# Kernel tuning notes

Hardware: AMD Instinct MI355X
Metric: run time of the kernel (lower is better)

## Reference

```python
import jax, jax.numpy as jnp
import numpy as np
import math

B, SEQ_LEN, LABEL_LEN, PRED_LEN = 32, 512, 256, 256
D_MODEL, N_HEADS, D_FF = 512, 8, 2048
ENC_IN, DEC_IN, C_OUT, MARK = 21, 21, 21, 4
MA_K, E_LAYERS, D_LAYERS, FACTOR = 25, 2, 1, 1
DEC_LEN = LABEL_LEN + PRED_LEN


def moving_mean(x, k):
    # replicate-pad front/back then avg-pool(kernel=k, stride=1); x: [B,L,C]
    pad = (k - 1) // 2
    xp = jnp.concatenate([jnp.repeat(x[:, :1], pad, axis=1), x,
                          jnp.repeat(x[:, -1:], pad, axis=1)], axis=1)
    cs = jnp.cumsum(xp, axis=1)
    cs = jnp.concatenate([jnp.zeros_like(cs[:, :1]), cs], axis=1)
    return (cs[:, k:] - cs[:, :-k]) / k


def series_decomp(x):
    trend = moving_mean(x, MA_K)
    return x - trend, trend


def circ_conv3(x, W):
    # circular-padded Conv1d kernel=3, no bias; x: [B,L,Cin], W: [3,Cin,Cout]
    xp = jnp.concatenate([x[:, -1:], x, x[:, :1]], axis=1)
    return xp[:, :-2] @ W[0] + xp[:, 1:-1] @ W[1] + xp[:, 2:] @ W[2]


def pos_embed(L, d):
    pos = jnp.arange(L, dtype=jnp.float32)[:, None]
    div = jnp.exp(jnp.arange(0, d, 2, dtype=jnp.float32) * (-math.log(10000.0) / d))
    pe = jnp.zeros((L, d), jnp.float32)
    pe = pe.at[:, 0::2].set(jnp.sin(pos * div)).at[:, 1::2].set(jnp.cos(pos * div))
    return pe


def data_embed(x, x_mark, val_W, time_W):
    # TokenEmbedding (circular conv) + TimeFeatureEmbedding (linear) + PositionalEmbedding
    return circ_conv3(x, val_W) + x_mark @ time_W + pos_embed(x.shape[1], D_MODEL)[None]


def autocorrelation(q, k, v):
    # q: [B,L,H,E]; k,v: [B,S,H,E]  -> [B,L,H,E]
    Bq, L, H, E = q.shape
    S = k.shape[1]
    if L > S:
        pad = jnp.zeros((Bq, L - S, H, E), q.dtype)
        k = jnp.concatenate([k, pad], axis=1)
        v = jnp.concatenate([v, pad], axis=1)
    else:
        k, v = k[:, :L], v[:, :L]
    qf = jnp.fft.rfft(q.transpose(0, 2, 3, 1), axis=-1)
    kf = jnp.fft.rfft(k.transpose(0, 2, 3, 1), axis=-1)
    corr = jnp.fft.irfft(qf * jnp.conj(kf), n=L, axis=-1)   # [B,H,E,L]
    vals = v.transpose(0, 2, 3, 1)                          # [B,H,E,L]
    top_k = int(FACTOR * math.log(L))
    mean_corr = corr.mean(axis=(1, 2))                      # [B,L]
    weights, delay = jax.lax.top_k(mean_corr, top_k)        # [B,K]
    w = jax.nn.softmax(weights, axis=-1)
    # gather from doubled values == circular shift by delay
    idx = (jnp.arange(L)[None, None, :] + delay[:, :, None]) % L   # [B,K,L]
    pat = jnp.take_along_axis(vals[:, None], idx[:, :, None, None, :], axis=-1)  # [B,K,H,E,L]
    agg = jnp.einsum('bkhel,bk->bhel', pat, w)
    return agg.transpose(0, 3, 1, 2)


def ac_layer(qx, kx, vx, Wq, Wk, Wv, Wo):
    Bq, L, D = qx.shape
    dk = D // N_HEADS
    q = (qx @ Wq).reshape(Bq, L, N_HEADS, dk)
    k = (kx @ Wk).reshape(Bq, kx.shape[1], N_HEADS, dk)
    v = (vx @ Wv).reshape(Bq, vx.shape[1], N_HEADS, dk)
    return autocorrelation(q, k, v).reshape(Bq, L, D) @ Wo


def ffn(x, W1, W2):
    # Conv1d kernel=1 (no bias) pair == pointwise MLP
    return jax.nn.gelu(x @ W1, approximate=False) @ W2


def seasonal_ln(x, g, b):
    mu = x.mean(-1, keepdims=True)
    var = ((x - mu) ** 2).mean(-1, keepdims=True)
    xh = (x - mu) / jnp.sqrt(var + 1e-5) * g + b
    return xh - xh.mean(axis=1, keepdims=True)


def encoder_layer(x, Wq, Wk, Wv, Wo, W1, W2):
    x = x + ac_layer(x, x, x, Wq, Wk, Wv, Wo)
    x, _ = series_decomp(x)
    y = ffn(x, W1, W2)
    x, _ = series_decomp(x + y)
    return x


def decoder_layer(x, cross, sWq, sWk, sWv, sWo, cWq, cWk, cWv, cWo, W1, W2, trend_W):
    x = x + ac_layer(x, x, x, sWq, sWk, sWv, sWo)
    x, t1 = series_decomp(x)
    x = x + ac_layer(x, cross, cross, cWq, cWk, cWv, cWo)
    x, t2 = series_decomp(x)
    y = ffn(x, W1, W2)
    x, t3 = series_decomp(x + y)
    residual_trend = circ_conv3(t1 + t2 + t3, trend_W)   # [B,L,C_OUT]
    return x, residual_trend


def _forward(x_enc, x_mark_enc, x_dec, x_mark_dec,
             enc_val_W, enc_time_W, enc_Wq, enc_Wk, enc_Wv, enc_Wo, enc_W1, enc_W2,
             enc_norm_g, enc_norm_b, dec_val_W, dec_time_W,
             dec_sWq, dec_sWk, dec_sWv, dec_sWo, dec_cWq, dec_cWk, dec_cWv, dec_cWo,
             dec_W1, dec_W2, dec_trend_W, dec_norm_g, dec_norm_b, proj_W, proj_b):
    mean = jnp.repeat(x_enc.mean(axis=1, keepdims=True), PRED_LEN, axis=1)
    zeros = jnp.zeros((x_dec.shape[0], PRED_LEN, x_dec.shape[2]), x_enc.dtype)
    seasonal_init, trend_init = series_decomp(x_enc)
    trend_init = jnp.concatenate([trend_init[:, -LABEL_LEN:], mean], axis=1)
    seasonal_init = jnp.concatenate([seasonal_init[:, -LABEL_LEN:], zeros], axis=1)
    enc = data_embed(x_enc, x_mark_enc, enc_val_W, enc_time_W)
    for i in range(E_LAYERS):
        enc = encoder_layer(enc, enc_Wq[i], enc_Wk[i], enc_Wv[i], enc_Wo[i], enc_W1[i], enc_W2[i])
    enc = seasonal_ln(enc, enc_norm_g, enc_norm_b)
    dec = data_embed(seasonal_init, x_mark_dec, dec_val_W, dec_time_W)
    trend = trend_init
    for i in range(D_LAYERS):
        dec, rt = decoder_layer(dec, enc, dec_sWq[i], dec_sWk[i], dec_sWv[i], dec_sWo[i],
                                dec_cWq[i], dec_cWk[i], dec_cWv[i], dec_cWo[i],
                                dec_W1[i], dec_W2[i], dec_trend_W[i])
        trend = trend + rt
    dec = seasonal_ln(dec, dec_norm_g, dec_norm_b)
    dec_out = dec @ proj_W + proj_b + trend
    return dec_out[:, -PRED_LEN:]


def setup_inputs() -> dict:
    key = jax.random.key(0)
    it = iter(jax.random.split(key, 40))
    def rn(shape, s=1.0):
        return jax.random.normal(next(it), shape, jnp.float32) * s
    W = 0.02
    return {
        'x_enc': rn((B, SEQ_LEN, ENC_IN)),
        'x_mark_enc': rn((B, SEQ_LEN, MARK)),
        'x_dec': rn((B, DEC_LEN, DEC_IN)),
        'x_mark_dec': rn((B, DEC_LEN, MARK)),
        'enc_val_W': rn((3, ENC_IN, D_MODEL), W),
        'enc_time_W': rn((MARK, D_MODEL), W),
        'enc_Wq': rn((E_LAYERS, D_MODEL, D_MODEL), W),
        'enc_Wk': rn((E_LAYERS, D_MODEL, D_MODEL), W),
        'enc_Wv': rn((E_LAYERS, D_MODEL, D_MODEL), W),
        'enc_Wo': rn((E_LAYERS, D_MODEL, D_MODEL), W),
        'enc_W1': rn((E_LAYERS, D_MODEL, D_FF), W),
        'enc_W2': rn((E_LAYERS, D_FF, D_MODEL), W),
        'enc_norm_g': jnp.ones((D_MODEL,), jnp.float32),
        'enc_norm_b': jnp.zeros((D_MODEL,), jnp.float32),
        'dec_val_W': rn((3, DEC_IN, D_MODEL), W),
        'dec_time_W': rn((MARK, D_MODEL), W),
        'dec_sWq': rn((D_LAYERS, D_MODEL, D_MODEL), W),
        'dec_sWk': rn((D_LAYERS, D_MODEL, D_MODEL), W),
        'dec_sWv': rn((D_LAYERS, D_MODEL, D_MODEL), W),
        'dec_sWo': rn((D_LAYERS, D_MODEL, D_MODEL), W),
        'dec_cWq': rn((D_LAYERS, D_MODEL, D_MODEL), W),
        'dec_cWk': rn((D_LAYERS, D_MODEL, D_MODEL), W),
        'dec_cWv': rn((D_LAYERS, D_MODEL, D_MODEL), W),
        'dec_cWo': rn((D_LAYERS, D_MODEL, D_MODEL), W),
        'dec_W1': rn((D_LAYERS, D_MODEL, D_FF), W),
        'dec_W2': rn((D_LAYERS, D_FF, D_MODEL), W),
        'dec_trend_W': rn((D_LAYERS, 3, D_MODEL, C_OUT), W),
        'dec_norm_g': jnp.ones((D_MODEL,), jnp.float32),
        'dec_norm_b': jnp.zeros((D_MODEL,), jnp.float32),
        'proj_W': rn((D_MODEL, C_OUT), W),
        'proj_b': jnp.zeros((C_OUT,), jnp.float32),
    }


def reference(x_enc, x_mark_enc, x_dec, x_mark_dec,
              enc_val_W, enc_time_W, enc_Wq, enc_Wk, enc_Wv, enc_Wo, enc_W1, enc_W2,
              enc_norm_g, enc_norm_b, dec_val_W, dec_time_W,
              dec_sWq, dec_sWk, dec_sWv, dec_sWo, dec_cWq, dec_cWk, dec_cWv, dec_cWo,
              dec_W1, dec_W2, dec_trend_W, dec_norm_g, dec_norm_b, proj_W, proj_b):
    return _forward(x_enc, x_mark_enc, x_dec, x_mark_dec,
                    enc_val_W, enc_time_W, enc_Wq, enc_Wk, enc_Wv, enc_Wo, enc_W1, enc_W2,
                    enc_norm_g, enc_norm_b, dec_val_W, dec_time_W,
                    dec_sWq, dec_sWk, dec_sWv, dec_sWo, dec_cWq, dec_cWk, dec_cWv, dec_cWo,
                    dec_W1, dec_W2, dec_trend_W, dec_norm_g, dec_norm_b, proj_W, proj_b)
```

## Files before the change

### kernel.cpp

```cpp
#include <hip/hip_runtime.h>


typedef _Float16 h8 __attribute__((ext_vector_type(8)));
typedef _Float16 h4 __attribute__((ext_vector_type(4)));
typedef float f32x4 __attribute__((ext_vector_type(4)));

struct P12 { const float* p[12]; };
struct P4  { const float* p[4]; };

__device__ __forceinline__ float gelu_f(float x){
    return 0.5f * x * (1.0f + erff(x * 0.70710678118654752f));
}

__device__ __forceinline__ void gl_lds(const _Float16* gp, _Float16* lp) {
    __builtin_amdgcn_global_load_lds(
        (const __attribute__((address_space(1))) void*)gp,
        (__attribute__((address_space(3))) void*)lp, 16, 0, 0);
}

__global__ void zero_k(float* __restrict__ p, long n){
    long i = (long)blockIdx.x * 256 + threadIdx.x;
    if (i < n) p[i] = 0.f;
}

template<int EPI, int OUT>
__global__ __launch_bounds__(256)
void hgemm_k(const _Float16* __restrict__ A, int lda, int loA,
             const _Float16* __restrict__ Bm, int ldb, int loB,
             const float* __restrict__ R, void* __restrict__ Cv,
             int ldc, int loC, int K, int nph, float osc,
             long sA, long sB, long sC)
{
    __shared__ _Float16 As[128 * 64];
    __shared__ _Float16 Bs[128 * 64];
    const int bz = blockIdx.z;
    const int tid = threadIdx.x, lane = tid & 63, w = tid >> 6;
    const int wr = w >> 1, wc = w & 1;
    const _Float16* Ap = A + bz * sA + (long)(blockIdx.y * 128) * lda;
    const _Float16* Bp = Bm + bz * sB + (long)(blockIdx.x * 128) * ldb;

    const int swz = ((lane & 7) ^ ((lane >> 3) & 7)) * 8;
    const int rsub = w * 32 + (lane >> 3);
    const _Float16* ApT = Ap + (long)rsub * lda + swz;
    const _Float16* BpT = Bp + (long)rsub * ldb + swz;
    _Float16* AsT = As + w * 2048;
    _Float16* BsT = Bs + w * 2048;

    const int tpp = K >> 6;
    const int nkt = tpp * nph;
    f32x4 acc[4][4] = {};

    int p = 0, q = 0;
    for (int kt = 0; kt < nkt; ++kt) {
        const int aoff = q * 64 + (p == 2 ? loA : 0);
        const int boff = q * 64 + (p == 1 ? loB : 0);
        __syncthreads();
#pragma unroll
        for (int i = 0; i < 4; i++) {
            gl_lds(ApT + (long)i * 8 * lda + aoff, AsT + i * 512);
            gl_lds(BpT + (long)i * 8 * ldb + boff, BsT + i * 512);
        }
        __syncthreads();
#pragma unroll
        for (int kk = 0; kk < 2; ++kk) {
            h8 af[4], bf[4];
            const int ks = kk * 4 + (lane >> 4);
#pragma unroll
            for (int m = 0; m < 4; m++) {
                int rowa = wr * 64 + m * 16 + (lane & 15);
                af[m] = *(const h8*)(As + rowa * 64 + ((ks ^ (rowa & 7)) * 8));
                int rowb = wc * 64 + m * 16 + (lane & 15);
                bf[m] = *(const h8*)(Bs + rowb * 64 + ((ks ^ (rowb & 7)) * 8));
            }
#pragma unroll
            for (int m = 0; m < 4; m++)
#pragma unroll
                for (int n = 0; n < 4; n++)
                    acc[m][n] = __builtin_amdgcn_mfma_f32_16x16x32_f16(af[m], bf[n], acc[m][n], 0, 0, 0);
        }
        if (++q == tpp) { q = 0; ++p; }
    }

    const int crow0 = blockIdx.y * 128 + wr * 64 + (lane >> 4) * 4;
    const int ccol0 = blockIdx.x * 128 + wc * 64 + (lane & 15);
    if constexpr (OUT == 0) {
        float* Cp = (float*)Cv + (long)bz * sC;
        const float* Rp = (EPI == 1) ? (R + (long)bz * sC) : nullptr;
#pragma unroll
        for (int m = 0; m < 4; m++)
#pragma unroll
            for (int n = 0; n < 4; n++) {
                int col = ccol0 + n * 16;
#pragma unroll
                for (int r2 = 0; r2 < 4; r2++) {
                    long idx = (long)(crow0 + m * 16 + r2) * ldc + col;
                    float v = acc[m][n][r2] * osc;
                    if (EPI == 1) v += Rp[idx];
                    Cp[idx] = v;
                }
            }
    } else if constexpr (OUT == 1) {
        _Float16* Cp = (_Float16*)Cv + (long)bz * sC;
#pragma unroll
        for (int m = 0; m < 4; m++)
#pragma unroll
            for (int n = 0; n < 4; n++) {
                int col = ccol0 + n * 16;
#pragma unroll
                for (int r2 = 0; r2 < 4; r2++) {
                    long base = (long)(crow0 + m * 16 + r2) * ldc + col;
                    float v = acc[m][n][r2] * osc;
                    if (EPI == 2) v = gelu_f(v);
                    _Float16 hi = (_Float16)v;
                    Cp[base] = hi;
                    if (loC >= 0) Cp[base + loC] = (_Float16)(v - (float)hi);
                }
            }
    } else {
        __shared__ float diag[512];
        float* mc = (float*)Cv + (long)bz * sC;
        for (int t = tid; t < 512; t += 256) diag[t] = 0.f;
        __syncthreads();
#pragma unroll
        for (int m = 0; m < 4; m++)
#pragma unroll
            for (int n = 0; n < 4; n++) {
                int col = ccol0 + n * 16;
#pragma unroll
                for (int r2 = 0; r2 < 4; r2++) {
                    int row = crow0 + m * 16 + r2;
                    atomicAdd(&diag[(row - col) & 511], acc[m][n][r2]);
                }
            }
        __syncthreads();
        for (int t = tid; t < 512; t += 256) {
            float v = diag[t];
            if (v != 0.f) atomicAdd(&mc[t], v);
        }
    }
}

__global__ __launch_bounds__(256)
void splitAll_k(P12 ps, _Float16* __restrict__ PA, _Float16* __restrict__ PB)
{
    const int m = blockIdx.y;
    const float* __restrict__ src = ps.p[m];
    _Float16* dst;
    if (m < 4)      dst = PA + (long)(2 * m) * 524288;
    else if (m < 8) dst = PB + (long)(2 * (m - 4)) * 524288;
    else            dst = PB + (long)(2 * (m - 8) + 1) * 524288;
    long t = (long)blockIdx.x * 256 + threadIdx.x;
    long row = t >> 6; int kc = (int)(t & 63) * 8;
    const float4 v0 = *(const float4*)(src + row * 512 + kc);
    const float4 v1 = *(const float4*)(src + row * 512 + kc + 4);
    float vv[8] = {v0.x,v0.y,v0.z,v0.w,v1.x,v1.y,v1.z,v1.w};
    h8 hi, lo;
#pragma unroll
    for (int j = 0; j < 8; j++) {
        float s = vv[j] * 64.f;
        _Float16 h = (_Float16)s;
        hi[j] = h; lo[j] = (_Float16)(s - (float)h);
    }
    *(h8*)(dst + row * 1024 + kc)       = hi;
    *(h8*)(dst + row * 1024 + 512 + kc) = lo;
}

__global__ __launch_bounds__(256)
void convWoAll_k(P4 ps, _Float16* __restrict__ PA)
{
    const int z = blockIdx.z;
    const float* __restrict__ src = ps.p[z];
    _Float16* dst = PA + (long)(2 * z + 1) * 524288;
    __shared__ float t[32][33];
    int k0 = blockIdx.x * 32, n0 = blockIdx.y * 32, tid = threadIdx.x;
#pragma unroll
    for (int i = 0; i < 4; i++) {
        int lin = tid + i * 256; int r = lin >> 5, c = lin & 31;
        t[r][c] = src[(long)(k0 + r) * 512 + n0 + c];
    }
    __syncthreads();
#pragma unroll
    for (int i = 0; i < 4; i++) {
        int lin = tid + i * 256; int n = lin >> 5, k = lin & 31;
        float v = t[k][n] * 64.f;
        _Float16 hi = (_Float16)v;
        long base = (long)(n0 + n) * 1024 + k0 + k;
        dst[base]       = hi;
        dst[base + 512] = (_Float16)(v - (float)hi);
    }
}

__global__ __launch_bounds__(256)
void convW2_k(const float* __restrict__ src, _Float16* __restrict__ dst,
              int N, int K)
{
    __shared__ float t[32][33];
    int k0 = blockIdx.x * 32, n0 = blockIdx.y * 32, tid = threadIdx.x;
#pragma unroll
    for (int i = 0; i < 4; i++) {
        int lin = tid + i * 256; int r = lin >> 5, c = lin & 31;
        t[r][c] = src[(long)(k0 + r) * N + n0 + c];
    }
    __syncthreads();
#pragma unroll
    for (int i = 0; i < 4; i++) {
        int lin = tid + i * 256; int n = lin >> 5, k = lin & 31;
        float v = t[k][n];
        _Float16 hi = (_Float16)v;
        long base = (long)(n0 + n) * 2 * K + k0 + k;
        dst[base]     = hi;
        dst[base + K] = (_Float16)(v - (float)hi);
    }
}

__global__ void convW63_k(const float* __restrict__ W, _Float16* __restrict__ dst)
{
    int i = blockIdx.x * 256 + threadIdx.x;
    int k = i & 511, j = i >> 9;
    float v = (j < 63) ? 64.f * W[(long)(j / 21) * 10752 + (long)k * 21 + (j % 21)] : 0.f;
    _Float16 hi = (_Float16)v;
    dst[(long)j * 1024 + k]       = hi;
    dst[(long)j * 1024 + 512 + k] = (_Float16)(v - (float)hi);
}

__global__ __launch_bounds__(256)
void embed_k(const float* __restrict__ x, const float* __restrict__ mark,
             const float* __restrict__ valW, const float* __restrict__ timeW,
             float* __restrict__ out, _Float16* __restrict__ cat)
{
    const int lg = blockIdx.x, dh = blockIdx.y, b = blockIdx.z;
    const int tid = threadIdx.x;
    const int dd = dh * 256 + tid;
    const int l0 = lg * 8;
    __shared__ float xs[10][21];
    __shared__ float mk[8][4];
    if (tid < 210) {
        int r = tid / 21, c = tid % 21;
        int ll = (l0 - 1 + r + 512) & 511;
        xs[r][c] = x[((long)b * 512 + ll) * 21 + c];
    }
    if (tid >= 224 && tid < 256) {
        int t2 = tid - 224, il = t2 >> 2, m = t2 & 3;
        mk[il][m] = mark[((long)b * 512 + l0 + il) * 4 + m];
    }
    __syncthreads();
    float acc[8];
#pragma unroll
    for (int il = 0; il < 8; il++) acc[il] = 0.f;
    for (int t = 0; t < 3; t++)
        for (int c = 0; c < 21; c++) {
            float w = valW[(t * 21 + c) * 512 + dd];
#pragma unroll
            for (int il = 0; il < 8; il++)
                acc[il] = fmaf(xs[il + t][c], w, acc[il]);
        }
    for (int m = 0; m < 4; m++) {
        float w = timeW[m * 512 + dd];
#pragma unroll
        for (int il = 0; il < 8; il++)
            acc[il] = fmaf(mk[il][m], w, acc[il]);
    }
    const float freq = expf((float)(dd & ~1) * (-9.210340371976184f / 512.0f));
#pragma unroll
    for (int il = 0; il < 8; il++) {
        float ang = (float)(l0 + il) * freq;
        float pe = (dd & 1) ? cosf(ang) : sinf(ang);
        float v = acc[il] + pe;
        long row = (long)b * 512 + l0 + il;
        out[row * 512 + dd] = v;
        _Float16 hi = (_Float16)v;
        cat[row * 1024 + dd]       = hi;
        cat[row * 1024 + 512 + dd] = (_Float16)(v - (float)hi);
    }
}

template<int TREND, int CAT>
__global__ __launch_bounds__(256)
void decompW_k(const float* __restrict__ x, float* __restrict__ out,
               _Float16* __restrict__ cat, _Float16* __restrict__ tsc)
{
    long t = (long)blockIdx.x * 256 + threadIdx.x;
    long rowg = t >> 7; int d4 = (int)(t & 127) * 4;
    int lg = (int)(rowg & 63); long b = rowg >> 6;
    const int l0 = lg * 8;
    const float* xb = x + (b << 18);
    float s[8][4] = {};
    float xo[8][4];
#pragma unroll
    for (int rr = -12; rr <= 19; rr++) {
        int rc = l0 + rr; rc = rc < 0 ? 0 : (rc > 511 ? 511 : rc);
        float4 v = *(const float4*)(xb + ((long)rc << 9) + d4);
        float vv[4] = {v.x, v.y, v.z, v.w};
#pragma unroll
        for (int i = 0; i < 8; i++) {
            if (i >= rr - 12 && i <= rr + 12) {
#pragma unroll
                for (int j = 0; j < 4; j++) s[i][j] += vv[j];
            }
        }
        if (rr >= 0 && rr < 8) {
#pragma unroll
            for (int j = 0; j < 4; j++) xo[rr][j] = vv[j];
        }
    }
#pragma unroll
    for (int i = 0; i < 8; i++) {
        long row = b * 512 + l0 + i;
        float tr[4], ov[4];
#pragma unroll
        for (int j = 0; j < 4; j++) {
            tr[j] = s[i][j] * (1.f / 25.f);
            ov[j] = xo[i][j] - tr[j];
        }
        *(float4*)(out + row * 512 + d4) = make_float4(ov[0], ov[1], ov[2], ov[3]);
        if (CAT) {
            h4 hi, lo;
#pragma unroll
            for (int j = 0; j < 4; j++) {
                _Float16 h = (_Float16)ov[j];
                hi[j] = h; lo[j] = (_Float16)(ov[j] - (float)h);
            }
            *(h4*)(cat + row * 1024 + d4)       = hi;
            *(h4*)(cat + row * 1024 + 512 + d4) = lo;
        }
        if (TREND) {
            _Float16* tp = tsc + row * 1024 + d4;
            if (TREND == 1) {
                h4 th = *(h4*)tp, tl = *(h4*)(tp + 512);
#pragma unroll
                for (int j = 0; j < 4; j++) tr[j] += (float)th[j] + (float)tl[j];
            }
            h4 th2, tl2;
#pragma unroll
            for (int j = 0; j < 4; j++) {
                _Float16 h = (_Float16)tr[j];
                th2[j] = h; tl2[j] = (_Float16)(tr[j] - (float)h);
            }
            *(h4*)tp         = th2;
            *(h4*)(tp + 512) = tl2;
        }
    }
}

__global__ void meanseq_k(const float* __restrict__ x, float* __restrict__ xm, int total)
{
    int i = blockIdx.x * 256 + threadIdx.x;
    if (i >= total) return;
    int c = i % 21, b = i / 21;
    float s = 0.f;
    for (int l = 0; l < 512; l++) s += x[((long)b * 512 + l) * 21 + c];
    xm[i] = s * (1.f / 512.f);
}

__global__ void prep_k(const float* __restrict__ x, const float* __restrict__ xm,
                       float* __restrict__ sinit, float* __restrict__ tinit, int total)
{
    int i = blockIdx.x * 256 + threadIdx.x;
    if (i >= total) return;
    int c = i % 21, l = (i / 21) % 512, b = i / 10752;
    if (l < 256) {
        int lc = 256 + l;
        float s = 0.f;
        for (int j = -12; j <= 12; j++) {
            int ll = lc + j; ll = ll > 511 ? 511 : ll;
            s += x[((long)b * 512 + ll) * 21 + c];
        }
        float t = s * (1.f / 25.f);
        tinit[i] = t;
        sinit[i] = x[((long)b * 512 + lc) * 21 + c] - t;
    } else {
        sinit[i] = 0.f;
        tinit[i] = xm[b * 21 + c];
    }
}

__global__ __launch_bounds__(256)
void topk_k(float* __restrict__ mc, int* __restrict__ delays,
            float* __restrict__ wts)
{
    const float SCL = 1.f / (512.f * 4096.f);
    int b = blockIdx.x, tid = threadIdx.x;
    __shared__ float v[512];
    __shared__ float rv[256];
    __shared__ int   ri[256];
    __shared__ float selv[6];
    v[tid]       = mc[b * 512 + tid]       * SCL;
    v[tid + 256] = mc[b * 512 + tid + 256] * SCL;
    mc[b * 512 + tid] = 0.f;
    mc[b * 512 + tid + 256] = 0.f;
    __syncthreads();
    for (int p = 0; p < 6; p++) {
        float bv = v[tid]; int bi = tid;
        float v2 = v[tid + 256];
        if (v2 > bv) { bv = v2; bi = tid + 256; }
        rv[tid] = bv; ri[tid] = bi;
        __syncthreads();
        for (int s = 128; s > 0; s >>= 1) {
            if (tid < s) {
                float ov = rv[tid + s]; int oi = ri[tid + s];
                if (ov > rv[tid] || (ov == rv[tid] && oi < ri[tid])) {
                    rv[tid] = ov; ri[tid] = oi;
                }
            }
            __syncthreads();
        }
        if (tid == 0) { selv[p] = rv[0]; delays[b * 6 + p] = ri[0]; v[ri[0]] = -3.4e38f; }
        __syncthreads();
    }
    if (tid == 0) {
        float mx = selv[0];
        for (int p = 1; p < 6; p++) mx = fmaxf(mx, selv[p]);
        float e[6], sum = 0.f;
        for (int p = 0; p < 6; p++) { e[p] = expf(selv[p] - mx); sum += e[p]; }
        for (int p = 0; p < 6; p++) wts[b * 6 + p] = e[p] / sum;
    }
}

__global__ __launch_bounds__(256)
void agg2_k(const _Float16* __restrict__ Vc, int vld,
            const int* __restrict__ delays, const float* __restrict__ wts,
            _Float16* __restrict__ out)
{
    long t = (long)blockIdx.x * 256 + threadIdx.x;
    int dc = (int)(t & 63);
    long row = t >> 6;
    int l = (int)(row & 511), b = (int)(row >> 9);
    float s[8] = {};
#pragma unroll
    for (int k = 0; k < 6; k++) {
        int dl = delays[b * 6 + k];
        float wv = wts[b * 6 + k];
        long sr = ((long)b * 512 + ((l + dl) & 511)) * vld + dc * 8;
        h8 hi8 = *(const h8*)(Vc + sr);
#pragma unroll
        for (int j = 0; j < 8; j++)
            s[j] = fmaf(wv, (float)hi8[j], s[j]);
    }
    h8 ho;
#pragma unroll
    for (int j = 0; j < 8; j++) ho[j] = (_Float16)s[j];
    *(h8*)(out + row * 512 + dc * 8) = ho;
}

__global__ __launch_bounds__(256)
void ln_k(const float* __restrict__ x, const float* __restrict__ g,
          const float* __restrict__ be, float* __restrict__ out)
{
    int row = blockIdx.x, tid = threadIdx.x;
    const float* xr = x + ((long)row << 9);
    float v0 = xr[tid], v1 = xr[tid + 256];
    __shared__ float rs[256];
    rs[tid] = v0 + v1; __syncthreads();
    for (int s = 128; s > 0; s >>= 1) { if (tid < s) rs[tid] += rs[tid + s]; __syncthreads(); }
    float mu = rs[0] * (1.f / 512.f);
    __syncthreads();
    float d0 = v0 - mu, d1 = v1 - mu;
    rs[tid] = d0 * d0 + d1 * d1; __syncthreads();
    for (int s = 128; s > 0; s >>= 1) { if (tid < s) rs[tid] += rs[tid + s]; __syncthreads(); }
    float rstd = 1.0f / sqrtf(rs[0] * (1.f / 512.f) + 1e-5f);
    out[((long)row << 9) + tid]       = d0 * rstd * g[tid] + be[tid];
    out[((long)row << 9) + tid + 256] = d1 * rstd * g[tid + 256] + be[tid + 256];
}

__global__ __launch_bounds__(256)
void colsum_k(const float* __restrict__ x, float* __restrict__ cs)
{
    int d = blockIdx.x * 256 + threadIdx.x;
    int b = blockIdx.y;
    const float* xb = x + ((long)b << 18);
    float s = 0.f;
    for (int l = 0; l < 512; l++) s += xb[((long)l << 9) + d];
    cs[((long)b << 9) + d] = s;
}

__global__ __launch_bounds__(256)
void subcolcat_k(const float* __restrict__ x, const float* __restrict__ cs,
                 _Float16* __restrict__ cat)
{
    long t = (long)blockIdx.x * 256 + threadIdx.x;
    long row = t >> 6; int d8 = (int)(t & 63) * 8;
    int b = (int)(row >> 9);
    const float4* c4 = (const float4*)(cs + ((long)b << 9) + d8);
    float4 m0 = c4[0], m1 = c4[1];
    float m[8] = {m0.x,m0.y,m0.z,m0.w,m1.x,m1.y,m1.z,m1.w};
    const float4* xp = (const float4*)(x + row * 512 + d8);
    float4 x0 = xp[0], x1 = xp[1];
    float v[8] = {x0.x,x0.y,x0.z,x0.w,x1.x,x1.y,x1.z,x1.w};
    h8 hi, lo;
#pragma unroll
    for (int j = 0; j < 8; j++) {
        float vv = v[j] - m[j] * (1.f / 512.f);
        _Float16 h = (_Float16)vv;
        hi[j] = h; lo[j] = (_Float16)(vv - (float)h);
    }
    *(h8*)(cat + row * 1024 + d8)       = hi;
    *(h8*)(cat + row * 1024 + 512 + d8) = lo;
}

__global__ void proj_k(const float* __restrict__ x, const float* __restrict__ cs,
                       const float* __restrict__ pw, const float* __restrict__ pb,
                       const float* __restrict__ tinit, const float* __restrict__ H,
                       float* __restrict__ out, int total)
{
    int i = blockIdx.x * 256 + threadIdx.x;
    if (i >= total) return;
    int c = i % 21, l = (i / 21) % 256 + 256, b = i / 5376;
    const float* xr = x + ((long)(b * 512 + l) << 9);
    const float* csb = cs + ((long)b << 9);
    float s = 0.f;
    for (int d = 0; d < 512; d++)
        s = fmaf(xr[d] - csb[d] * (1.f / 512.f), pw[d * 21 + c], s);
    long r = (long)b * 512;
    float trend = tinit[b * 10752 + l * 21 + c]
                + H[(r + ((l + 511) & 511)) * 128 + c]
                + H[(r + l) * 128 + 21 + c]
                + H[(r + ((l + 1) & 511)) * 128 + 42 + c];
    out[i] = s + pb[c] + trend;
}

static void hgemm(int mode, int nph, float osc,
                  const _Float16* A, int lda, int loA,
                  const _Float16* B, int ldb, int loB,
                  const float* R, void* C, int ldc, int loC,
                  int K, int M, int N, int batch,
                  long sA, long sB, long sC, hipStream_t st)
{
    dim3 g(N / 128, M / 128, batch), blk(256);
    switch (mode) {
    case 0:  hgemm_k<0,1><<<g,blk,0,st>>>(A,lda,loA,B,ldb,loB,R,C,ldc,loC,K,nph,osc,sA,sB,sC); break;
    case 2:  hgemm_k<2,1><<<g,blk,0,st>>>(A,lda,loA,B,ldb,loB,R,C,ldc,loC,K,nph,osc,sA,sB,sC); break;
    case 10: hgemm_k<1,0><<<g,blk,0,st>>>(A,lda,loA,B,ldb,loB,R,C,ldc,loC,K,nph,osc,sA,sB,sC); break;
    case 11: hgemm_k<0,0><<<g,blk,0,st>>>(A,lda,loA,B,ldb,loB,R,C,ldc,loC,K,nph,osc,sA,sB,sC); break;
    default: hgemm_k<0,2><<<g,blk,0,st>>>(A,lda,loA,B,ldb,loB,R,C,ldc,loC,K,nph,osc,sA,sB,sC); break;
    }
}

extern "C" void kernel_launch(void* const* d_in, const int* in_sizes, int n_in,
                              void* d_out, int out_size, void* d_ws, size_t ws_size,
                              hipStream_t stream)
{
    const float* x_enc    = (const float*)d_in[0];
    const float* xm_enc   = (const float*)d_in[1];
    const float* xm_dec   = (const float*)d_in[3];
    const float* enc_valW = (const float*)d_in[4];
    const float* enc_timeW= (const float*)d_in[5];
    const float* enc_Wq   = (const float*)d_in[6];
    const float* enc_Wk   = (const float*)d_in[7];
    const float* enc_Wv   = (const float*)d_in[8];
    const float* enc_Wo   = (const float*)d_in[9];
    const float* enc_W1   = (const float*)d_in[10];
    const float* enc_W2   = (const float*)d_in[11];
    const float* enc_g    = (const float*)d_in[12];
    const float* enc_b    = (const float*)d_in[13];
    const float* dec_valW = (const float*)d_in[14];
    const float* dec_timeW= (const float*)d_in[15];
    const float* sWq = (const float*)d_in[16];
    const float* sWk = (const float*)d_in[17];
    const float* sWv = (const float*)d_in[18];
    const float* sWo = (const float*)d_in[19];
    const float* cWq = (const float*)d_in[20];
    const float* cWk = (const float*)d_in[21];
    const float* cWv = (const float*)d_in[22];
    const float* cWo = (const float*)d_in[23];
    const float* dW1 = (const float*)d_in[24];
    const float* dW2 = (const float*)d_in[25];
    const float* dtW = (const float*)d_in[26];
    const float* dec_g = (const float*)d_in[27];
    const float* dec_b = (const float*)d_in[28];
    const float* projW = (const float*)d_in[29];
    const float* projB = (const float*)d_in[30];

    const size_t W_BYTES = 50000000;
    const size_t perB = 8900000;
    int Bc = 32;
    while (Bc > 1 && W_BYTES + (size_t)Bc * perB + (4u << 20) > ws_size) Bc >>= 1;

    char* wp = (char*)d_ws;
    auto alloc = [&](size_t bytes) { char* p = wp; wp += (bytes + 255) & ~(size_t)255; return p; };

    _Float16* Wcat8  = (_Float16*)alloc(8 * 524288 * 2);
    _Float16* encW1C = (_Float16*)alloc(2 * 2097152 * 2);
    _Float16* encW2C = (_Float16*)alloc(2 * 2097152 * 2);
    _Float16* dW1C   = (_Float16*)alloc(2097152 * 2);
    _Float16* dW2C   = (_Float16*)alloc(2097152 * 2);
    _Float16* W63C   = (_Float16*)alloc(131072 * 2);
    _Float16* PA     = (_Float16*)alloc(8 * 524288 * 2);
    _Float16* PB     = (_Float16*)alloc(8 * 524288 * 2);

    const long ROWS = (long)Bc * 512;
    const long NBc  = ROWS * 512;
    float*    X      = (float*)alloc(NBc * 4);
    float*    O      = (float*)alloc(NBc * 4);
    _Float16* TSc    = (_Float16*)alloc(ROWS * 1024 * 2);
    _Float16* cX     = (_Float16*)alloc(ROWS * 1024 * 2);
    _Float16* cAgg   = (_Float16*)alloc(ROWS * 512 * 2);
    _Float16* ENCcat = (_Float16*)alloc(ROWS * 1024 * 2);
    _Float16* bigcat = (_Float16*)alloc(ROWS * 2048 * 2);
    float* H       = (float*)alloc(ROWS * 128 * 4);
    float* sinit   = (float*)alloc((long)Bc * 10752 * 4);
    float* tinit   = (float*)alloc((long)Bc * 10752 * 4);
    float* xmean   = (float*)alloc((long)Bc * 21 * 4);
    float* mc      = (float*)alloc((long)Bc * 512 * 4);
    float* cs      = (float*)alloc((long)Bc * 512 * 4);
    float* wts     = (float*)alloc((long)Bc * 6 * 4);
    int*   delays  = (int*)alloc((long)Bc * 6 * 4);

    dim3 cb(256);
    P12 sp;
    sp.p[0] = enc_Wk;           sp.p[1] = enc_Wk + 262144;
    sp.p[2] = sWk;              sp.p[3] = cWk;
    sp.p[4] = enc_Wq;           sp.p[5] = enc_Wq + 262144;
    sp.p[6] = sWq;              sp.p[7] = cWq;
    sp.p[8] = enc_Wv;           sp.p[9] = enc_Wv + 262144;
    sp.p[10] = sWv;             sp.p[11] = cWv;
    P4 op;
    op.p[0] = enc_Wo;           op.p[1] = enc_Wo + 262144;
    op.p[2] = sWo;              op.p[3] = cWo;
    splitAll_k <<<dim3(128,12), cb, 0, stream>>>(sp, PA, PB);
    convWoAll_k<<<dim3(16,16,4), cb, 0, stream>>>(op, PA);
    hgemm(0, 3, 1.f, PA,1024,512, PB,1024,512, nullptr, Wcat8, 1024, 512,
          512, 512, 512, 8, 524288, 524288, 524288, stream);
    for (int L = 0; L < 2; L++) {
        convW2_k<<<dim3(16,64), cb, 0, stream>>>(enc_W1 + (long)L*1048576, encW1C + (long)L*2097152, 2048, 512);
        convW2_k<<<dim3(64,16), cb, 0, stream>>>(enc_W2 + (long)L*1048576, encW2C + (long)L*2097152, 512, 2048);
    }
    convW2_k<<<dim3(16,64), cb, 0, stream>>>(dW1, dW1C, 2048, 512);
    convW2_k<<<dim3(64,16), cb, 0, stream>>>(dW2, dW2C, 512, 2048);
    convW63_k<<<256, cb, 0, stream>>>(dtW, W63C);

    const int M = (int)ROWS;
    const int t21 = Bc * 10752;
    const int gRows = Bc * 128;
    const int gW = Bc * 32;
    const long sCA = 512 * 1024;
    const float IOS = 1.f / 4096.f;

    zero_k<<<(Bc*512 + 255)/256, 256, 0, stream>>>(mc, Bc*512);

    auto attn = [&](float* Xin, float* Cout, const _Float16* cQ,
                    const _Float16* KVcat, int slot) {
        const _Float16* WqkC_ = Wcat8 + (long)(2*slot)     * 524288;
        const _Float16* WvoC_ = Wcat8 + (long)(2*slot + 1) * 524288;
        hgemm(0, 3, 1.f, cQ,1024,512, WqkC_,1024,512, nullptr, bigcat, 1024, 512,
              512, M, 512, 1, 0,0,0, stream);
        hgemm(20, 3, 1.f, bigcat,1024,512, KVcat,1024,512, nullptr, mc, 0, 0,
              512, 512, 512, Bc, sCA, sCA, 512, stream);
        topk_k<<<Bc, 256, 0, stream>>>(mc, delays, wts);
        agg2_k<<<gRows, 256, 0, stream>>>(KVcat, 1024, delays, wts, cAgg);
        hgemm(10, 1, IOS, cAgg,512,0, WvoC_,1024,512, Xin, Cout, 512, 0,
              512, M, 512, 1, 0,0,0, stream);
    };
    auto ffn = [&](float* Xin, float* Cout, const _Float16* cXin,
                   const _Float16* W1C, const _Float16* W2C) {
        hgemm(2, 1, 1.f, cXin,1024,512, W1C,1024,512, nullptr, bigcat, 2048, -1,
              512, M, 2048, 1, 0,0,0, stream);
        hgemm(10, 1, 1.f, bigcat,2048,0, W2C,4096,2048, Xin, Cout, 512, 0,
              2048, M, 512, 1, 0,0,0, stream);
    };

    for (int b0 = 0; b0 < 32; b0 += Bc) {
        const float* xe  = x_enc  + (long)b0 * 10752;
        const float* mke = xm_enc + (long)b0 * 2048;
        const float* mkd = xm_dec + (long)b0 * 2048;
        float* outp = (float*)d_out + (long)b0 * 5376;

        meanseq_k<<<(Bc*21 + 255)/256, 256, 0, stream>>>(xe, xmean, Bc*21);
        prep_k   <<<(t21 + 255)/256, 256, 0, stream>>>(xe, xmean, sinit, tinit, t21);

        embed_k<<<dim3(64,2,Bc), 256, 0, stream>>>(xe, mke, enc_valW, enc_timeW, X, cX);
        for (int L = 0; L < 2; L++) {
            attn(X, O, cX, cX, L);
            decompW_k<0,1><<<gW, 256, 0, stream>>>(O, X, cX, nullptr);
            ffn(X, O, cX, encW1C + (long)L*2097152, encW2C + (long)L*2097152);
            decompW_k<0,1><<<gW, 256, 0, stream>>>(O, X, cX, nullptr);
        }
        ln_k      <<<Bc*512, 256, 0, stream>>>(X, enc_g, enc_b, O);
        colsum_k  <<<dim3(2,Bc), 256, 0, stream>>>(O, cs);
        subcolcat_k<<<gRows, 256, 0, stream>>>(O, cs, ENCcat);

        embed_k<<<dim3(64,2,Bc), 256, 0, stream>>>(sinit, mkd, dec_valW, dec_timeW, X, cX);

        attn(X, O, cX, cX, 2);
        decompW_k<2,1><<<gW, 256, 0, stream>>>(O, X, cX, TSc);

        attn(X, O, cX, ENCcat, 3);
        decompW_k<1,1><<<gW, 256, 0, stream>>>(O, X, cX, TSc);

        ffn(X, O, cX, dW1C, dW2C);
        decompW_k<1,0><<<gW, 256, 0, stream>>>(O, X, nullptr, TSc);

        hgemm(11, 1, 1.f/64.f, TSc,1024,512, W63C,1024,512, nullptr, H, 128, 0,
              512, M, 128, 1, 0,0,0, stream);
        ln_k      <<<Bc*512, 256, 0, stream>>>(X, dec_g, dec_b, O);
        colsum_k  <<<dim3(2,Bc), 256, 0, stream>>>(O, cs);
        proj_k    <<<(Bc*5376+255)/256, 256, 0, stream>>>(O, cs, projW, projB,
                                                          tinit, H, outp, Bc*5376);
    }
}
```

Baseline: 2.213 ms.

## Store residual stream as split fp16 hi/lo pairs instead of fp32

Replaces the fp32 residual buffers X/O with hi/lo fp16 pair buffers, so GEMM epilogues add the residual from the pair form and write pairs directly, and decomposition and layernorm read pairs. This removes the duplicate fp32 write alongside the fp16 copy and shrinks per-batch workspace, which may allow larger batch chunks. It also replaces the serial per-channel mean kernel with a block-parallel reduction. Precision of the residual is preserved approximately via the hi+lo split.

```diff
diff --git a/kernel.cpp b/kernel.cpp
--- a/kernel.cpp
+++ b/kernel.cpp
@@ -27,7 +27,7 @@
 __global__ __launch_bounds__(256)
 void hgemm_k(const _Float16* __restrict__ A, int lda, int loA,
              const _Float16* __restrict__ Bm, int ldb, int loB,
-             const float* __restrict__ R, void* __restrict__ Cv,
+             const _Float16* __restrict__ Rc, void* __restrict__ Cv,
              int ldc, int loC, int K, int nph, float osc,
              long sA, long sB, long sC)
 {
@@ -85,7 +85,6 @@
     const int ccol0 = blockIdx.x * 128 + wc * 64 + (lane & 15);
     if constexpr (OUT == 0) {
         float* Cp = (float*)Cv + (long)bz * sC;
-        const float* Rp = (EPI == 1) ? (R + (long)bz * sC) : nullptr;
 #pragma unroll
         for (int m = 0; m < 4; m++)
 #pragma unroll
@@ -94,9 +93,7 @@
 #pragma unroll
                 for (int r2 = 0; r2 < 4; r2++) {
                     long idx = (long)(crow0 + m * 16 + r2) * ldc + col;
-                    float v = acc[m][n][r2] * osc;
-                    if (EPI == 1) v += Rp[idx];
-                    Cp[idx] = v;
+                    Cp[idx] = acc[m][n][r2] * osc;
                 }
             }
     } else if constexpr (OUT == 1) {
@@ -108,8 +105,13 @@
                 int col = ccol0 + n * 16;
 #pragma unroll
                 for (int r2 = 0; r2 < 4; r2++) {
-                    long base = (long)(crow0 + m * 16 + r2) * ldc + col;
+                    int row = crow0 + m * 16 + r2;
+                    long base = (long)row * ldc + col;
                     float v = acc[m][n][r2] * osc;
+                    if (EPI == 1) {
+                        long rb = (long)row * 1024 + col;
+                        v += (float)Rc[rb] + (float)Rc[rb + 512];
+                    }
                     if (EPI == 2) v = gelu_f(v);
                     _Float16 hi = (_Float16)v;
                     Cp[base] = hi;
@@ -226,7 +228,7 @@
 __global__ __launch_bounds__(256)
 void embed_k(const float* __restrict__ x, const float* __restrict__ mark,
              const float* __restrict__ valW, const float* __restrict__ timeW,
-             float* __restrict__ out, _Float16* __restrict__ cat)
+             _Float16* __restrict__ cat)
 {
     const int lg = blockIdx.x, dh = blockIdx.y, b = blockIdx.z;
     const int tid = threadIdx.x;
@@ -267,30 +269,32 @@
         float pe = (dd & 1) ? cosf(ang) : sinf(ang);
         float v = acc[il] + pe;
         long row = (long)b * 512 + l0 + il;
-        out[row * 512 + dd] = v;
         _Float16 hi = (_Float16)v;
         cat[row * 1024 + dd]       = hi;
         cat[row * 1024 + 512 + dd] = (_Float16)(v - (float)hi);
     }
 }
 
-template<int TREND, int CAT>
-__global__ __launch_bounds__(256)
-void decompW_k(const float* __restrict__ x, float* __restrict__ out,
-               _Float16* __restrict__ cat, _Float16* __restrict__ tsc)
+template<int TREND>
+__global__ __launch_bounds__(256)
+void decompW_k(const _Float16* __restrict__ xc, _Float16* __restrict__ outc,
+               _Float16* __restrict__ tsc)
 {
     long t = (long)blockIdx.x * 256 + threadIdx.x;
     long rowg = t >> 7; int d4 = (int)(t & 127) * 4;
     int lg = (int)(rowg & 63); long b = rowg >> 6;
     const int l0 = lg * 8;
-    const float* xb = x + (b << 18);
+    const _Float16* xb = xc + (b << 19);
     float s[8][4] = {};
     float xo[8][4];
 #pragma unroll
     for (int rr = -12; rr <= 19; rr++) {
         int rc = l0 + rr; rc = rc < 0 ? 0 : (rc > 511 ? 511 : rc);
-        float4 v = *(const float4*)(xb + ((long)rc << 9) + d4);
-        float vv[4] = {v.x, v.y, v.z, v.w};
+        h4 vh = *(const h4*)(xb + ((long)rc << 10) + d4);
+        h4 vl = *(const h4*)(xb + ((long)rc << 10) + 512 + d4);
+        float vv[4];
+#pragma unroll
+        for (int j = 0; j < 4; j++) vv[j] = (float)vh[j] + (float)vl[j];
 #pragma unroll
         for (int i = 0; i < 8; i++) {
             if (i >= rr - 12 && i <= rr + 12) {
@@ -312,17 +316,14 @@
             tr[j] = s[i][j] * (1.f / 25.f);
             ov[j] = xo[i][j] - tr[j];
         }
-        *(float4*)(out + row * 512 + d4) = make_float4(ov[0], ov[1], ov[2], ov[3]);
-        if (CAT) {
-            h4 hi, lo;
-#pragma unroll
-            for (int j = 0; j < 4; j++) {
-                _Float16 h = (_Float16)ov[j];
-                hi[j] = h; lo[j] = (_Float16)(ov[j] - (float)h);
-            }
-            *(h4*)(cat + row * 1024 + d4)       = hi;
-            *(h4*)(cat + row * 1024 + 512 + d4) = lo;
-        }
+        h4 hi, lo;
+#pragma unroll
+        for (int j = 0; j < 4; j++) {
+            _Float16 h = (_Float16)ov[j];
+            hi[j] = h; lo[j] = (_Float16)(ov[j] - (float)h);
+        }
+        *(h4*)(outc + row * 1024 + d4)       = hi;
+        *(h4*)(outc + row * 1024 + 512 + d4) = lo;
         if (TREND) {
             _Float16* tp = tsc + row * 1024 + d4;
             if (TREND == 1) {
@@ -342,14 +343,26 @@
     }
 }
 
-__global__ void meanseq_k(const float* __restrict__ x, float* __restrict__ xm, int total)
-{
-    int i = blockIdx.x * 256 + threadIdx.x;
-    if (i >= total) return;
-    int c = i % 21, b = i / 21;
-    float s = 0.f;
-    for (int l = 0; l < 512; l++) s += x[((long)b * 512 + l) * 21 + c];
-    xm[i] = s * (1.f / 512.f);
+__global__ __launch_bounds__(512)
+void meanseq2_k(const float* __restrict__ x, float* __restrict__ xm)
+{
+    int b = blockIdx.x, tid = threadIdx.x;
+    __shared__ float sd[504];
+    if (tid < 504) {
+        int c = tid % 21, g = tid / 21;
+        int l0 = g * 22, l1 = l0 + 22 > 512 ? 512 : l0 + 22;
+        const float* xb = x + (long)b * 10752;
+        float s = 0.f;
+        for (int l = l0; l < l1; l++) s += xb[l * 21 + c];
+        sd[tid] = s;
+    }
+    __syncthreads();
+    if (tid < 21) {
+        float t = 0.f;
+#pragma unroll
+        for (int g = 0; g < 24; g++) t += sd[g * 21 + tid];
+        xm[b * 21 + tid] = t * (1.f / 512.f);
+    }
 }
 
 __global__ void prep_k(const float* __restrict__ x, const float* __restrict__ xm,
@@ -443,12 +456,13 @@
 }
 
 __global__ __launch_bounds__(256)
-void ln_k(const float* __restrict__ x, const float* __restrict__ g,
+void ln_k(const _Float16* __restrict__ xc, const float* __restrict__ g,
           const float* __restrict__ be, float* __restrict__ out)
 {
     int row = blockIdx.x, tid = threadIdx.x;
-    const float* xr = x + ((long)row << 9);
-    float v0 = xr[tid], v1 = xr[tid + 256];
+    const _Float16* xr = xc + ((long)row << 10);
+    float v0 = (float)xr[tid]       + (float)xr[tid + 512];
+    float v1 = (float)xr[tid + 256] + (float)xr[tid + 768];
     __shared__ float rs[256];
     rs[tid] = v0 + v1; __syncthreads();
     for (int s = 128; s > 0; s >>= 1) { if (tid < s) rs[tid] += rs[tid + s]; __syncthreads(); }
@@ -521,17 +535,17 @@
 static void hgemm(int mode, int nph, float osc,
                   const _Float16* A, int lda, int loA,
                   const _Float16* B, int ldb, int loB,
-                  const float* R, void* C, int ldc, int loC,
+                  const _Float16* Rc, void* C, int ldc, int loC,
                   int K, int M, int N, int batch,
                   long sA, long sB, long sC, hipStream_t st)
 {
     dim3 g(N / 128, M / 128, batch), blk(256);
     switch (mode) {
-    case 0:  hgemm_k<0,1><<<g,blk,0,st>>>(A,lda,loA,B,ldb,loB,R,C,ldc,loC,K,nph,osc,sA,sB,sC); break;
-    case 2:  hgemm_k<2,1><<<g,blk,0,st>>>(A,lda,loA,B,ldb,loB,R,C,ldc,loC,K,nph,osc,sA,sB,sC); break;
-    case 10: hgemm_k<1,0><<<g,blk,0,st>>>(A,lda,loA,B,ldb,loB,R,C,ldc,loC,K,nph,osc,sA,sB,sC); break;
-    case 11: hgemm_k<0,0><<<g,blk,0,st>>>(A,lda,loA,B,ldb,loB,R,C,ldc,loC,K,nph,osc,sA,sB,sC); break;
-    default: hgemm_k<0,2><<<g,blk,0,st>>>(A,lda,loA,B,ldb,loB,R,C,ldc,loC,K,nph,osc,sA,sB,sC); break;
+    case 0:  hgemm_k<0,1><<<g,blk,0,st>>>(A,lda,loA,B,ldb,loB,Rc,C,ldc,loC,K,nph,osc,sA,sB,sC); break;
+    case 2:  hgemm_k<2,1><<<g,blk,0,st>>>(A,lda,loA,B,ldb,loB,Rc,C,ldc,loC,K,nph,osc,sA,sB,sC); break;
+    case 12: hgemm_k<1,1><<<g,blk,0,st>>>(A,lda,loA,B,ldb,loB,Rc,C,ldc,loC,K,nph,osc,sA,sB,sC); break;
+    case 11: hgemm_k<0,0><<<g,blk,0,st>>>(A,lda,loA,B,ldb,loB,Rc,C,ldc,loC,K,nph,osc,sA,sB,sC); break;
+    default: hgemm_k<0,2><<<g,blk,0,st>>>(A,lda,loA,B,ldb,loB,Rc,C,ldc,loC,K,nph,osc,sA,sB,sC); break;
     }
 }
 
@@ -571,7 +585,7 @@
     const float* projB = (const float*)d_in[30];
 
     const size_t W_BYTES = 50000000;
-    const size_t perB = 8900000;
+    const size_t perB = 8400000;
     int Bc = 32;
     while (Bc > 1 && W_BYTES + (size_t)Bc * perB + (4u << 20) > ws_size) Bc >>= 1;
 
@@ -588,14 +602,13 @@
     _Float16* PB     = (_Float16*)alloc(8 * 524288 * 2);
 
     const long ROWS = (long)Bc * 512;
-    const long NBc  = ROWS * 512;
-    float*    X      = (float*)alloc(NBc * 4);
-    float*    O      = (float*)alloc(NBc * 4);
+    _Float16* cX     = (_Float16*)alloc(ROWS * 1024 * 2);
+    _Float16* cO     = (_Float16*)alloc(ROWS * 1024 * 2);
     _Float16* TSc    = (_Float16*)alloc(ROWS * 1024 * 2);
-    _Float16* cX     = (_Float16*)alloc(ROWS * 1024 * 2);
     _Float16* cAgg   = (_Float16*)alloc(ROWS * 512 * 2);
     _Float16* ENCcat = (_Float16*)alloc(ROWS * 1024 * 2);
     _Float16* bigcat = (_Float16*)alloc(ROWS * 2048 * 2);
+    float* F       = (float*)alloc(ROWS * 512 * 4);
     float* H       = (float*)alloc(ROWS * 128 * 4);
     float* sinit   = (float*)alloc((long)Bc * 10752 * 4);
     float* tinit   = (float*)alloc((long)Bc * 10752 * 4);
@@ -607,15 +620,15 @@
 
     dim3 cb(256);
     P12 sp;
-    sp.p[0] = enc_Wk;           sp.p[1] = enc_Wk + 262144;
-    sp.p[2] = sWk;              sp.p[3] = cWk;
-    sp.p[4] = enc_Wq;           sp.p[5] = enc_Wq + 262144;
-    sp.p[6] = sWq;              sp.p[7] = cWq;
-    sp.p[8] = enc_Wv;           sp.p[9] = enc_Wv + 262144;
-    sp.p[10] = sWv;             sp.p[11] = cWv;
+    sp.p[0] = enc_Wk;  sp.p[1] = enc_Wk + 262144;
+    sp.p[2] = sWk;     sp.p[3] = cWk;
+    sp.p[4] = enc_Wq;  sp.p[5] = enc_Wq + 262144;
+    sp.p[6] = sWq;     sp.p[7] = cWq;
+    sp.p[8] = enc_Wv;  sp.p[9] = enc_Wv + 262144;
+    sp.p[10] = sWv;    sp.p[11] = cWv;
     P4 op;
-    op.p[0] = enc_Wo;           op.p[1] = enc_Wo + 262144;
-    op.p[2] = sWo;              op.p[3] = cWo;
+    op.p[0] = enc_Wo;  op.p[1] = enc_Wo + 262144;
+    op.p[2] = sWo;     op.p[3] = cWo;
     splitAll_k <<<dim3(128,12), cb, 0, stream>>>(sp, PA, PB);
     convWoAll_k<<<dim3(16,16,4), cb, 0, stream>>>(op, PA);
     hgemm(0, 3, 1.f, PA,1024,512, PB,1024,512, nullptr, Wcat8, 1024, 512,
@@ -637,24 +650,24 @@
 
     zero_k<<<(Bc*512 + 255)/256, 256, 0, stream>>>(mc, Bc*512);
 
-    auto attn = [&](float* Xin, float* Cout, const _Float16* cQ,
+    auto attn = [&](const _Float16* cIn, _Float16* cOut,
                     const _Float16* KVcat, int slot) {
         const _Float16* WqkC_ = Wcat8 + (long)(2*slot)     * 524288;
         const _Float16* WvoC_ = Wcat8 + (long)(2*slot + 1) * 524288;
-        hgemm(0, 3, 1.f, cQ,1024,512, WqkC_,1024,512, nullptr, bigcat, 1024, 512,
+        hgemm(0, 3, 1.f, cIn,1024,512, WqkC_,1024,512, nullptr, bigcat, 1024, 512,
               512, M, 512, 1, 0,0,0, stream);
         hgemm(20, 3, 1.f, bigcat,1024,512, KVcat,1024,512, nullptr, mc, 0, 0,
               512, 512, 512, Bc, sCA, sCA, 512, stream);
         topk_k<<<Bc, 256, 0, stream>>>(mc, delays, wts);
         agg2_k<<<gRows, 256, 0, stream>>>(KVcat, 1024, delays, wts, cAgg);
-        hgemm(10, 1, IOS, cAgg,512,0, WvoC_,1024,512, Xin, Cout, 512, 0,
+        hgemm(12, 1, IOS, cAgg,512,0, WvoC_,1024,512, cIn, cOut, 1024, 512,
               512, M, 512, 1, 0,0,0, stream);
     };
-    auto ffn = [&](float* Xin, float* Cout, const _Float16* cXin,
+    auto ffn = [&](const _Float16* cIn, _Float16* cOut,
                    const _Float16* W1C, const _Float16* W2C) {
-        hgemm(2, 1, 1.f, cXin,1024,512, W1C,1024,512, nullptr, bigcat, 2048, -1,
+        hgemm(2, 1, 1.f, cIn,1024,512, W1C,1024,512, nullptr, bigcat, 2048, -1,
               512, M, 2048, 1, 0,0,0, stream);
-        hgemm(10, 1, 1.f, bigcat,2048,0, W2C,4096,2048, Xin, Cout, 512, 0,
+        hgemm(12, 1, 1.f, bigcat,2048,0, W2C,4096,2048, cIn, cOut, 1024, 512,
               2048, M, 512, 1, 0,0,0, stream);
     };
 
@@ -664,36 +677,34 @@
         const float* mkd = xm_dec + (long)b0 * 2048;
         float* outp = (float*)d_out + (long)b0 * 5376;
 
-        meanseq_k<<<(Bc*21 + 255)/256, 256, 0, stream>>>(xe, xmean, Bc*21);
-        prep_k   <<<(t21 + 255)/256, 256, 0, stream>>>(xe, xmean, sinit, tinit, t21);
-
-        embed_k<<<dim3(64,2,Bc), 256, 0, stream>>>(xe, mke, enc_valW, enc_timeW, X, cX);
+        meanseq2_k<<<Bc, 512, 0, stream>>>(xe, xmean);
+        prep_k    <<<(t21 + 255)/256, 256, 0, stream>>>(xe, xmean, sinit, tinit, t21);
+
+        embed_k<<<dim3(64,2,Bc), 256, 0, stream>>>(xe, mke, enc_valW, enc_timeW, cX);
         for (int L = 0; L < 2; L++) {
-            attn(X, O, cX, cX, L);
-            decompW_k<0,1><<<gW, 256, 0, stream>>>(O, X, cX, nullptr);
-            ffn(X, O, cX, encW1C + (long)L*2097152, encW2C + (long)L*2097152);
-            decompW_k<0,1><<<gW, 256, 0, stream>>>(O, X, cX, nullptr);
-        }
-        ln_k      <<<Bc*512, 256, 0, stream>>>(X, enc_g, enc_b, O);
-        colsum_k  <<<dim3(2,Bc), 256, 0, stream>>>(O, cs);
-        subcolcat_k<<<gRows, 256, 0, stream>>>(O, cs, ENCcat);
-
-        embed_k<<<dim3(64,2,Bc), 256, 0, stream>>>(sinit, mkd, dec_valW, dec_timeW, X, cX);
-
-        attn(X, O, cX, cX, 2);
-        decompW_k<2,1><<<gW, 256, 0, stream>>>(O, X, cX, TSc);
-
-        attn(X, O, cX, ENCcat, 3);
-        decompW_k<1,1><<<gW, 256, 0, stream>>>(O, X, cX, TSc);
-
-        ffn(X, O, cX, dW1C, dW2C);
-        decompW_k<1,0><<<gW, 256, 0, stream>>>(O, X, nullptr, TSc);
+            attn(cX, cO, cX, L);
+            decompW_k<0><<<gW, 256, 0, stream>>>(cO, cX, nullptr);
+            ffn(cX, cO, encW1C + (long)L*2097152, encW2C + (long)L*2097152);
+            decompW_k<0><<<gW, 256, 0, stream>>>(cO, cX, nullptr);
+        }
+        ln_k       <<<Bc*512, 256, 0, stream>>>(cX, enc_g, enc_b, F);
+        colsum_k   <<<dim3(2,Bc), 256, 0, stream>>>(F, cs);
+        subcolcat_k<<<gRows, 256, 0, stream>>>(F, cs, ENCcat);
+
+        embed_k<<<dim3(64,2,Bc), 256, 0, stream>>>(sinit, mkd, dec_valW, dec_timeW, cX);
+
+        attn(cX, cO, cX, 2);
+        decompW_k<2><<<gW, 256, 0, stream>>>(cO, cX, TSc);
+        attn(cX, cO, ENCcat, 3);
+        decompW_k<1><<<gW, 256, 0, stream>>>(cO, cX, TSc);
+        ffn(cX, cO, dW1C, dW2C);
+        decompW_k<1><<<gW, 256, 0, stream>>>(cO, cX, TSc);
 
         hgemm(11, 1, 1.f/64.f, TSc,1024,512, W63C,1024,512, nullptr, H, 128, 0,
               512, M, 128, 1, 0,0,0, stream);
-        ln_k      <<<Bc*512, 256, 0, stream>>>(X, dec_g, dec_b, O);
-        colsum_k  <<<dim3(2,Bc), 256, 0, stream>>>(O, cs);
-        proj_k    <<<(Bc*5376+255)/256, 256, 0, stream>>>(O, cs, projW, projB,
-                                                          tinit, H, outp, Bc*5376);
-    }
-}
+        ln_k    <<<Bc*512, 256, 0, stream>>>(cX, dec_g, dec_b, F);
+        colsum_k<<<dim3(2,Bc), 256, 0, stream>>>(F, cs);
+        proj_k  <<<(Bc*5376+255)/256, 256, 0, stream>>>(F, cs, projW, projB,
+                                                        tinit, H, outp, Bc*5376);
+    }
+}
```

Result: no change. 2.233 ms (+0.9%).
